# Kernel optimization log

Measured on AMD Instinct MI355X. Metric: run time of the kernel, lower is better.

## Reference

```python
import jax, jax.numpy as jnp
import numpy as np

B, N, NH, E_IN = 2, 2048, 32, 128   # batch, grid cells, neighborhood size, input feat
MD, H, FF, OUT = 512, 8, 2048, 128  # model_dim, heads, ff_dim, output_dim
HD = MD // H                        # head dim = 64
PED, TABLE = 32, 512                # pos_emb_dim, number of (distance,phi) bins
EPS = 1e-5


def setup_inputs() -> dict:
    key = jax.random.key(0)
    ks = jax.random.split(key, 16)
    def w(k, shp, s=0.02):
        return jax.random.normal(k, shp, jnp.float32) * s
    return {
        "x": jax.random.normal(ks[0], (B, N, NH, E_IN), jnp.float32),
        "distances": jax.random.randint(ks[1], (B * N, NH, NH), 0, TABLE),
        "phis": jax.random.randint(ks[2], (B * N, NH, NH), 0, TABLE),
        "W_in": w(ks[3], (E_IN, MD)),
        "dist_table": w(ks[4], (TABLE, PED), 1.0),
        "phi_table": w(ks[5], (TABLE, PED), 1.0),
        "W_bias": w(ks[6], (PED, H)),
        "Wq": w(ks[7], (MD, MD)),
        "Wk": w(ks[8], (MD, MD)),
        "Wv": w(ks[9], (MD, MD)),
        "Wo": w(ks[10], (MD, MD)),
        "W_ff1": w(ks[11], (MD, FF)),
        "W_ff2": w(ks[12], (FF, MD)),
        "g1": jnp.ones((MD,), jnp.float32),
        "b1": jnp.zeros((MD,), jnp.float32),
        "g2": jnp.ones((MD,), jnp.float32),
        "b2": jnp.zeros((MD,), jnp.float32),
        "W_out": w(ks[13], (MD, OUT)),
    }


def _layernorm(x, g, b):
    m = x.mean(-1, keepdims=True)
    v = ((x - m) ** 2).mean(-1, keepdims=True)
    return (x - m) * jax.lax.rsqrt(v + EPS) * g + b


def reference(x, distances, phis, W_in, dist_table, phi_table, W_bias,
              Wq, Wk, Wv, Wo, W_ff1, W_ff2, g1, b1, g2, b2, W_out):
    b, n, nh, _ = x.shape
    m = b * n
    # input_mlp (bias-free Linear), fold (b, n) into batch of attention problems
    h = (x @ W_in).reshape(m, nh, MD)                       # [m, nh, MD]
    # relative position bias: emb_table lookup, product, Linear(PED -> H)
    pe = dist_table[distances] * phi_table[phis]            # [m, nh, nh, PED]
    bias = jnp.einsum('mijp,ph->mhij', pe, W_bias)          # [m, H, nh, nh]
    # MHA with qkv projections (bias-free)
    q = (h @ Wq).reshape(m, nh, H, HD).transpose(0, 2, 1, 3)
    k = (h @ Wk).reshape(m, nh, H, HD).transpose(0, 2, 1, 3)
    v = (h @ Wv).reshape(m, nh, H, HD).transpose(0, 2, 1, 3)
    scores = jnp.einsum('mhid,mhjd->mhij', q, k) / np.sqrt(HD).astype(np.float32)
    att = jax.nn.softmax(scores + bias, axis=-1)            # [m, H, nh, nh]
    o = jnp.einsum('mhij,mhjd->mhid', att, v)
    att_out = o.transpose(0, 2, 1, 3).reshape(m, nh, MD) @ Wo
    # q_res residual (dropout=0), LayerNorm, FFN (SiLU), LayerNorm
    h1 = _layernorm(h + att_out, g1, b1)
    ff = jax.nn.silu(h1 @ W_ff1) @ W_ff2
    h2 = _layernorm(h1 + ff, g2, b2)
    # unfold and output_mlp
    return h2.reshape(b, n, nh, MD) @ W_out                 # [b, n, nh, OUT]
```

## Files before the change

### kernel.cpp

```cpp
#include <hip/hip_runtime.h>
#include <hip/hip_bf16.h>
#include <cstdint>
#include <cstddef>

typedef __bf16 bf16;
typedef __bf16 bf16x8 __attribute__((ext_vector_type(8)));
typedef float  f32x4  __attribute__((ext_vector_type(4)));
typedef float  f32x16 __attribute__((ext_vector_type(16)));

#define DEVI static __device__ __forceinline__

DEVI float ldf(const void* p, size_t i, bool isbf) {
  return isbf ? (float)((const bf16*)p)[i] : ((const float*)p)[i];
}

__global__ void probe_dtype(const void* w, int* flag) {
  int tid = threadIdx.x;
  const bf16* p = (const bf16*)w;
  float mx = 0.f;
  for (int i = tid; i < 2048; i += 64) {
    float v = fabsf((float)p[i]);
    if (!(v < 1e30f)) v = 1e30f;
    mx = fmaxf(mx, v);
  }
#pragma unroll
  for (int d = 32; d; d >>= 1) mx = fmaxf(mx, __shfl_xor(mx, d, 64));
  if (tid == 0) *flag = (mx < 100.f) ? 1 : 0;
}

__global__ void convert_bf16(const void* src, size_t eoff, bf16* dst, int n,
                             const int* flag) {
  int i = (blockIdx.x * 256 + threadIdx.x) * 8;
  if (i >= n) return;
  if (*flag) {
    *(uint4*)(dst + i) = *(const uint4*)((const bf16*)src + eoff + i);
  } else {
    const float* s = (const float*)src + eoff + i;
    float4 a = *(const float4*)s;
    float4 b = *(const float4*)(s + 4);
    bf16 o[8] = {(bf16)a.x, (bf16)a.y, (bf16)a.z, (bf16)a.w,
                 (bf16)b.x, (bf16)b.y, (bf16)b.z, (bf16)b.w};
    *(uint4*)(dst + i) = *(const uint4*)o;
  }
}

__global__ void transpose_w(const void* W, bf16* WT, int K, int N, const int* flag) {
  int idx = blockIdx.x * 256 + threadIdx.x;
  if (idx >= K * N) return;
  int n = idx / K, k = idx - n * K;
  WT[idx] = (bf16)ldf(W, (size_t)k * N + n, *flag != 0);
}

__global__ __launch_bounds__(256) void build_F(const void* dt, const void* pt,
                                               const void* Wb, bf16* F,
                                               const int* flag) {
  int pair = blockIdx.x * 256 + threadIdx.x;
  int d = pair >> 9, ph = pair & 511;
  bool isbf = (*flag != 0);
  float acc[8] = {0, 0, 0, 0, 0, 0, 0, 0};
#pragma unroll
  for (int p = 0; p < 32; ++p) {
    float pe = ldf(dt, (size_t)d * 32 + p, isbf) * ldf(pt, (size_t)ph * 32 + p, isbf);
#pragma unroll
    for (int hh = 0; hh < 8; ++hh) acc[hh] += pe * ldf(Wb, (size_t)p * 8 + hh, isbf);
  }
#pragma unroll
  for (int hh = 0; hh < 8; ++hh) F[(size_t)pair * 8 + hh] = (bf16)acc[hh];
}

__global__ __launch_bounds__(256) void build_bias(const int* __restrict__ dist,
                                                  const int* __restrict__ phi,
                                                  const bf16* __restrict__ F,
                                                  bf16* __restrict__ bias) {
  const int m = blockIdx.x;
#pragma unroll
  for (int it = 0; it < 4; ++it) {
    int e = it * 256 + threadIdx.x;
    int d = dist[(size_t)m * 1024 + e];
    int ph = phi[(size_t)m * 1024 + e];
    uint4 fv = *(const uint4*)(F + ((size_t)d * 512 + ph) * 8);
    const bf16* fe = (const bf16*)&fv;
#pragma unroll
    for (int hh = 0; hh < 8; ++hh)
      bias[((size_t)m * 8 + hh) * 1024 + e] = fe[hh];
  }
}

template <int DO_SILU, int OUT_DUAL>
__global__ __launch_bounds__(256) void gemm_bt(const bf16* __restrict__ A,
                                               const bf16* __restrict__ BT,
                                               void* __restrict__ Cv, int N, int K,
                                               const int* flag, size_t row0) {
  __shared__ bf16 As[128 * 32];
  __shared__ bf16 Bs[128 * 32];
  const int bn = blockIdx.x * 128;
  const int bm = blockIdx.y * 128;
  const int tid = threadIdx.x;
  const int lane = tid & 63;
  const int wave = tid >> 6;
  const int wr = (wave >> 1) * 64, wc = (wave & 1) * 64;
  const int srow = tid >> 2, skk = (tid & 3) * 8;
  const size_t sK = (size_t)K;
  const int kq = (lane >> 4) * 8;
  const int fr = lane & 15;
  f32x4 acc[4][4] = {};
  for (int k0 = 0; k0 < K; k0 += 32) {
    bf16x8 a0 = *(const bf16x8*)(A + (size_t)(bm + srow) * sK + k0 + skk);
    bf16x8 a1 = *(const bf16x8*)(A + (size_t)(bm + 64 + srow) * sK + k0 + skk);
    bf16x8 b0 = *(const bf16x8*)(BT + (size_t)(bn + srow) * sK + k0 + skk);
    bf16x8 b1 = *(const bf16x8*)(BT + (size_t)(bn + 64 + srow) * sK + k0 + skk);
    __syncthreads();
    *(bf16x8*)(As + srow * 32 + skk) = a0;
    *(bf16x8*)(As + (64 + srow) * 32 + skk) = a1;
    *(bf16x8*)(Bs + srow * 32 + skk) = b0;
    *(bf16x8*)(Bs + (64 + srow) * 32 + skk) = b1;
    __syncthreads();
    bf16x8 af[4], bfr[4];
#pragma unroll
    for (int i = 0; i < 4; ++i)
      af[i] = *(const bf16x8*)(As + (wr + i * 16 + fr) * 32 + kq);
#pragma unroll
    for (int j = 0; j < 4; ++j)
      bfr[j] = *(const bf16x8*)(Bs + (wc + j * 16 + fr) * 32 + kq);
#pragma unroll
    for (int i = 0; i < 4; ++i)
#pragma unroll
      for (int j = 0; j < 4; ++j)
        acc[i][j] = __builtin_amdgcn_mfma_f32_16x16x32_bf16(af[i], bfr[j], acc[i][j], 0, 0, 0);
  }
  const int fq = (lane >> 4) * 4;
  const bool write_f32 = OUT_DUAL && flag && (*flag == 0);
#pragma unroll
  for (int i = 0; i < 4; ++i)
#pragma unroll
    for (int j = 0; j < 4; ++j)
#pragma unroll
      for (int r = 0; r < 4; ++r) {
        size_t row = row0 + (size_t)(bm + wr + i * 16 + fq + r);
        size_t col = (size_t)(bn + wc + j * 16 + fr);
        float v = acc[i][j][r];
        if (DO_SILU) v = v / (1.f + __expf(-v));
        if (OUT_DUAL && write_f32)
          ((float*)Cv)[row * N + col] = v;
        else
          ((bf16*)Cv)[row * N + col] = (bf16)v;
      }
}

__global__ __launch_bounds__(512) void attn_fused(const bf16* __restrict__ QKV,
                                                  const bf16* __restrict__ bias,
                                                  bf16* __restrict__ O) {
  const int m = blockIdx.x;
  const int lane = threadIdx.x & 63;
  const int h = threadIdx.x >> 6;
  __shared__ bf16 Vs[8][32 * 64];
  __shared__ bf16 Ps[8][32 * 32];
  const size_t rowbase = (size_t)m * 32 * 1536;
#pragma unroll
  for (int rr = 0; rr < 4; ++rr) {
    int e = rr * 512 + lane * 8;
    int i = e >> 6, c = e & 63;
    *(uint4*)&Vs[h][e] =
        *(const uint4*)(QKV + rowbase + (size_t)i * 1536 + 1024 + h * 64 + c);
  }
  const int fr = lane & 31;
  const int kq = (lane >> 5) * 8;
  bf16x8 qf[4], kf[4];
#pragma unroll
  for (int kk = 0; kk < 4; ++kk) {
    qf[kk] = *(const bf16x8*)(QKV + rowbase + (size_t)fr * 1536 + h * 64 + kk * 16 + kq);
    kf[kk] = *(const bf16x8*)(QKV + rowbase + (size_t)fr * 1536 + 512 + h * 64 + kk * 16 + kq);
  }
  f32x16 s = {};
#pragma unroll
  for (int kk = 0; kk < 4; ++kk)
    s = __builtin_amdgcn_mfma_f32_32x32x16_bf16(qf[kk], kf[kk], s, 0, 0, 0);
  const bf16* bp = bias + ((size_t)m * 8 + h) * 1024;
  const int ri = 4 * (lane >> 5);
  float p[16];
#pragma unroll
  for (int r = 0; r < 16; ++r) {
    int i = (r & 3) + 8 * (r >> 2) + ri;
    p[r] = s[r] * 0.125f + (float)bp[i * 32 + fr];
  }
#pragma unroll
  for (int r = 0; r < 16; ++r) {
    float mx = p[r];
#pragma unroll
    for (int d = 16; d; d >>= 1) mx = fmaxf(mx, __shfl_xor(mx, d, 64));
    float e = __expf(p[r] - mx);
    float sum = e;
#pragma unroll
    for (int d = 16; d; d >>= 1) sum += __shfl_xor(sum, d, 64);
    p[r] = e / sum;
  }
#pragma unroll
  for (int r = 0; r < 16; ++r) {
    int i = (r & 3) + 8 * (r >> 2) + ri;
    Ps[h][i * 32 + fr] = (bf16)p[r];
  }
  __syncthreads();
  bf16x8 pf[2];
#pragma unroll
  for (int kk = 0; kk < 2; ++kk)
    pf[kk] = *(const bf16x8*)(&Ps[h][fr * 32 + kk * 16 + kq]);
  f32x16 o0 = {}, o1 = {};
#pragma unroll
  for (int kk = 0; kk < 2; ++kk) {
    bf16x8 v0, v1;
#pragma unroll
    for (int e = 0; e < 8; ++e) {
      v0[e] = Vs[h][(kk * 16 + kq + e) * 64 + fr];
      v1[e] = Vs[h][(kk * 16 + kq + e) * 64 + 32 + fr];
    }
    o0 = __builtin_amdgcn_mfma_f32_32x32x16_bf16(pf[kk], v0, o0, 0, 0, 0);
    o1 = __builtin_amdgcn_mfma_f32_32x32x16_bf16(pf[kk], v1, o1, 0, 0, 0);
  }
  bf16* op = O + (size_t)m * 32 * 512 + h * 64;
#pragma unroll
  for (int r = 0; r < 16; ++r) {
    int i = (r & 3) + 8 * (r >> 2) + ri;
    op[(size_t)i * 512 + fr] = (bf16)o0[r];
    op[(size_t)i * 512 + 32 + fr] = (bf16)o1[r];
  }
}

__global__ __launch_bounds__(256) void ln_fused(const bf16* __restrict__ X,
                                                const bf16* __restrict__ Y,
                                                const bf16* __restrict__ gb, int gboff,
                                                bf16* __restrict__ out) {
  const int row = blockIdx.x * 4 + (threadIdx.x >> 6);
  const int lane = threadIdx.x & 63;
  uint4 xr = *(const uint4*)(X + (size_t)row * 512 + lane * 8);
  uint4 yr = *(const uint4*)(Y + (size_t)row * 512 + lane * 8);
  const bf16* xe = (const bf16*)&xr;
  const bf16* ye = (const bf16*)&yr;
  float v[8];
  float sum = 0.f;
#pragma unroll
  for (int e = 0; e < 8; ++e) { v[e] = (float)xe[e] + (float)ye[e]; sum += v[e]; }
#pragma unroll
  for (int d = 32; d; d >>= 1) sum += __shfl_xor(sum, d, 64);
  float mean = sum * (1.f / 512.f);
  float var = 0.f;
#pragma unroll
  for (int e = 0; e < 8; ++e) { float t = v[e] - mean; var += t * t; }
#pragma unroll
  for (int d = 32; d; d >>= 1) var += __shfl_xor(var, d, 64);
  float rstd = rsqrtf(var * (1.f / 512.f) + 1e-5f);
  uint4 gr = *(const uint4*)(gb + gboff + lane * 8);
  uint4 br = *(const uint4*)(gb + gboff + 512 + lane * 8);
  const bf16* ge = (const bf16*)&gr;
  const bf16* be = (const bf16*)&br;
  bf16 o[8];
#pragma unroll
  for (int e = 0; e < 8; ++e)
    o[e] = (bf16)((v[e] - mean) * rstd * (float)ge[e] + (float)be[e]);
  *(uint4*)(out + (size_t)row * 512 + lane * 8) = *(const uint4*)o;
}

extern "C" void kernel_launch(void* const* d_in, const int* in_sizes, int n_in,
                              void* d_out, int out_size, void* d_ws, size_t ws_size,
                              hipStream_t stream) {
  const int T = 131072;
  const void* x    = d_in[0];
  const int*  dist = (const int*)d_in[1];
  const int*  phiI = (const int*)d_in[2];
  const void* Win  = d_in[3];
  const void* dtab = d_in[4];
  const void* ptab = d_in[5];
  const void* Wb   = d_in[6];
  const void* Wq   = d_in[7];
  const void* Wk   = d_in[8];
  const void* Wv   = d_in[9];
  const void* Wo   = d_in[10];
  const void* Wf1  = d_in[11];
  const void* Wf2  = d_in[12];
  const void* g1   = d_in[13];
  const void* b1   = d_in[14];
  const void* g2   = d_in[15];
  const void* b2   = d_in[16];
  const void* Wout = d_in[17];
  (void)in_sizes; (void)n_in; (void)out_size;

  const size_t FIXED = (size_t)16 << 20;
  int R = 131072;
  while (R > 1024 && FIXED + (size_t)R * 7936 > ws_size) R >>= 1;
  const int MC = R / 32;
  const int NCHUNK = T / R;

  char* wsb = (char*)d_ws;
  size_t off = 0;
  auto alloc = [&](size_t bytes) {
    char* p = wsb + off;
    off += (bytes + 511) & ~(size_t)511;
    return p;
  };
  int*  flag = (int*)alloc(4);
  bf16* gb   = (bf16*)alloc(2048 * 2);
  bf16* WinT = (bf16*)alloc((size_t)512 * 128 * 2);
  bf16* QKVT = (bf16*)alloc((size_t)1536 * 512 * 2);
  bf16* WoT  = (bf16*)alloc((size_t)512 * 512 * 2);
  bf16* Wf1T = (bf16*)alloc((size_t)2048 * 512 * 2);
  bf16* Wf2T = (bf16*)alloc((size_t)512 * 2048 * 2);
  bf16* WouT = (bf16*)alloc((size_t)128 * 512 * 2);
  bf16* Ftab = (bf16*)alloc((size_t)262144 * 8 * 2);
  bf16* Xc   = (bf16*)alloc((size_t)R * 128 * 2);
  bf16* Hc   = (bf16*)alloc((size_t)R * 512 * 2);
  bf16* big  = (bf16*)alloc((size_t)R * 2048 * 2);
  bf16* Oc   = (bf16*)alloc((size_t)R * 512 * 2);
  bf16* AOc  = (bf16*)alloc((size_t)R * 512 * 2);
  bf16* biasc= (bf16*)alloc((size_t)MC * 8 * 1024 * 2);

  probe_dtype<<<1, 64, 0, stream>>>(Win, flag);
  convert_bf16<<<1, 256, 0, stream>>>(g1, 0, gb + 0, 512, flag);
  convert_bf16<<<1, 256, 0, stream>>>(b1, 0, gb + 512, 512, flag);
  convert_bf16<<<1, 256, 0, stream>>>(g2, 0, gb + 1024, 512, flag);
  convert_bf16<<<1, 256, 0, stream>>>(b2, 0, gb + 1536, 512, flag);
  transpose_w<<<(512 * 128 + 255) / 256, 256, 0, stream>>>(Win, WinT, 128, 512, flag);
  transpose_w<<<(512 * 512 + 255) / 256, 256, 0, stream>>>(Wq, QKVT, 512, 512, flag);
  transpose_w<<<(512 * 512 + 255) / 256, 256, 0, stream>>>(Wk, QKVT + 512 * 512, 512, 512, flag);
  transpose_w<<<(512 * 512 + 255) / 256, 256, 0, stream>>>(Wv, QKVT + 1024 * 512, 512, 512, flag);
  transpose_w<<<(512 * 512 + 255) / 256, 256, 0, stream>>>(Wo, WoT, 512, 512, flag);
  transpose_w<<<(2048 * 512 + 255) / 256, 256, 0, stream>>>(Wf1, Wf1T, 512, 2048, flag);
  transpose_w<<<(2048 * 512 + 255) / 256, 256, 0, stream>>>(Wf2, Wf2T, 2048, 512, flag);
  transpose_w<<<(128 * 512 + 255) / 256, 256, 0, stream>>>(Wout, WouT, 512, 128, flag);
  build_F<<<262144 / 256, 256, 0, stream>>>(dtab, ptab, Wb, Ftab, flag);

  dim3 blk(256);
  for (int c = 0; c < NCHUNK; ++c) {
    const size_t rowoff = (size_t)c * R;
    const size_t moff = (size_t)c * MC;
    convert_bf16<<<(R * 128 / 8 + 255) / 256, 256, 0, stream>>>(x, rowoff * 128, Xc, R * 128, flag);
    gemm_bt<0, 0><<<dim3(4, R / 128), blk, 0, stream>>>(Xc, WinT, Hc, 512, 128, nullptr, 0);
    gemm_bt<0, 0><<<dim3(12, R / 128), blk, 0, stream>>>(Hc, QKVT, big, 1536, 512, nullptr, 0);
    build_bias<<<MC, 256, 0, stream>>>(dist + moff * 1024, phiI + moff * 1024, Ftab, biasc);
    attn_fused<<<MC, 512, 0, stream>>>(big, biasc, Oc);
    gemm_bt<0, 0><<<dim3(4, R / 128), blk, 0, stream>>>(Oc, WoT, AOc, 512, 512, nullptr, 0);
    ln_fused<<<R / 4, 256, 0, stream>>>(Hc, AOc, gb, 0, Hc);
    gemm_bt<1, 0><<<dim3(16, R / 128), blk, 0, stream>>>(Hc, Wf1T, big, 2048, 512, nullptr, 0);
    gemm_bt<0, 0><<<dim3(4, R / 128), blk, 0, stream>>>(big, Wf2T, AOc, 512, 2048, nullptr, 0);
    ln_fused<<<R / 4, 256, 0, stream>>>(Hc, AOc, gb, 1024, Hc);
    gemm_bt<0, 1><<<dim3(1, R / 128), blk, 0, stream>>>(Hc, WouT, d_out, 128, 512, flag, rowoff);
  }
}
```

Before: 2.219 ms.

## Use direct global-to-LDS loads in GEMM and vectorize bias table build

The GEMM tile staging now uses global_load_lds to move A/B tiles straight into shared memory, skipping the register round-trip. The LDS layout relies on tid*8 matching srow*32+skk, which holds. Separately, build_F now reads from pre-converted fp32 tables through float4 loads, caches W_bias in LDS and writes packed 16-byte outputs. The GEMM is still single-buffered with two barriers per K step, so load latency stays exposed.

After: 2.216 ms. Within noise of the previous version (-0.1%).

```diff
diff --git a/kernel.cpp b/kernel.cpp
--- a/kernel.cpp
+++ b/kernel.cpp
@@ -9,6 +9,13 @@
 typedef float  f32x16 __attribute__((ext_vector_type(16)));
 
 #define DEVI static __device__ __forceinline__
+
+DEVI void gload_lds16(const void* g, void* l) {
+  __builtin_amdgcn_global_load_lds(
+      (const __attribute__((address_space(1))) uint32_t*)(uintptr_t)g,
+      (__attribute__((address_space(3))) uint32_t*)(uint32_t)(uintptr_t)l,
+      16, 0, 0);
+}
 
 DEVI float ldf(const void* p, size_t i, bool isbf) {
   return isbf ? (float)((const bf16*)p)[i] : ((const float*)p)[i];
@@ -44,6 +51,12 @@
   }
 }
 
+__global__ void convert_f32(const void* src, float* dst, int n, const int* flag) {
+  int i = blockIdx.x * 256 + threadIdx.x;
+  if (i >= n) return;
+  dst[i] = ldf(src, i, *flag != 0);
+}
+
 __global__ void transpose_w(const void* W, bf16* WT, int K, int N, const int* flag) {
   int idx = blockIdx.x * 256 + threadIdx.x;
   if (idx >= K * N) return;
@@ -51,21 +64,31 @@
   WT[idx] = (bf16)ldf(W, (size_t)k * N + n, *flag != 0);
 }
 
-__global__ __launch_bounds__(256) void build_F(const void* dt, const void* pt,
-                                               const void* Wb, bf16* F,
-                                               const int* flag) {
+__global__ __launch_bounds__(256) void build_F(const float* __restrict__ dt32,
+                                               const float* __restrict__ pt32,
+                                               const float* __restrict__ Wb32,
+                                               bf16* __restrict__ F) {
+  __shared__ float WbS[256];
+  WbS[threadIdx.x] = Wb32[threadIdx.x];
+  __syncthreads();
   int pair = blockIdx.x * 256 + threadIdx.x;
   int d = pair >> 9, ph = pair & 511;
-  bool isbf = (*flag != 0);
+  const float4* dtv = (const float4*)(dt32 + (size_t)d * 32);
+  const float4* ptv = (const float4*)(pt32 + (size_t)ph * 32);
   float acc[8] = {0, 0, 0, 0, 0, 0, 0, 0};
 #pragma unroll
-  for (int p = 0; p < 32; ++p) {
-    float pe = ldf(dt, (size_t)d * 32 + p, isbf) * ldf(pt, (size_t)ph * 32 + p, isbf);
-#pragma unroll
-    for (int hh = 0; hh < 8; ++hh) acc[hh] += pe * ldf(Wb, (size_t)p * 8 + hh, isbf);
-  }
-#pragma unroll
-  for (int hh = 0; hh < 8; ++hh) F[(size_t)pair * 8 + hh] = (bf16)acc[hh];
+  for (int q = 0; q < 8; ++q) {
+    float4 a = dtv[q], b = ptv[q];
+    float pe[4] = {a.x * b.x, a.y * b.y, a.z * b.z, a.w * b.w};
+#pragma unroll
+    for (int e = 0; e < 4; ++e)
+#pragma unroll
+      for (int hh = 0; hh < 8; ++hh) acc[hh] += pe[e] * WbS[(q * 4 + e) * 8 + hh];
+  }
+  bf16 o[8];
+#pragma unroll
+  for (int hh = 0; hh < 8; ++hh) o[hh] = (bf16)acc[hh];
+  *(uint4*)(F + (size_t)pair * 8) = *(const uint4*)o;
 }
 
 __global__ __launch_bounds__(256) void build_bias(const int* __restrict__ dist,
@@ -105,15 +128,11 @@
   const int fr = lane & 15;
   f32x4 acc[4][4] = {};
   for (int k0 = 0; k0 < K; k0 += 32) {
-    bf16x8 a0 = *(const bf16x8*)(A + (size_t)(bm + srow) * sK + k0 + skk);
-    bf16x8 a1 = *(const bf16x8*)(A + (size_t)(bm + 64 + srow) * sK + k0 + skk);
-    bf16x8 b0 = *(const bf16x8*)(BT + (size_t)(bn + srow) * sK + k0 + skk);
-    bf16x8 b1 = *(const bf16x8*)(BT + (size_t)(bn + 64 + srow) * sK + k0 + skk);
     __syncthreads();
-    *(bf16x8*)(As + srow * 32 + skk) = a0;
-    *(bf16x8*)(As + (64 + srow) * 32 + skk) = a1;
-    *(bf16x8*)(Bs + srow * 32 + skk) = b0;
-    *(bf16x8*)(Bs + (64 + srow) * 32 + skk) = b1;
+    gload_lds16(A + (size_t)(bm + srow) * sK + k0 + skk, As + tid * 8);
+    gload_lds16(A + (size_t)(bm + 64 + srow) * sK + k0 + skk, As + 2048 + tid * 8);
+    gload_lds16(BT + (size_t)(bn + srow) * sK + k0 + skk, Bs + tid * 8);
+    gload_lds16(BT + (size_t)(bn + 64 + srow) * sK + k0 + skk, Bs + 2048 + tid * 8);
     __syncthreads();
     bf16x8 af[4], bfr[4];
 #pragma unroll
@@ -298,6 +317,9 @@
   };
   int*  flag = (int*)alloc(4);
   bf16* gb   = (bf16*)alloc(2048 * 2);
+  float* dt32 = (float*)alloc((size_t)512 * 32 * 4);
+  float* pt32 = (float*)alloc((size_t)512 * 32 * 4);
+  float* Wb32 = (float*)alloc(256 * 4);
   bf16* WinT = (bf16*)alloc((size_t)512 * 128 * 2);
   bf16* QKVT = (bf16*)alloc((size_t)1536 * 512 * 2);
   bf16* WoT  = (bf16*)alloc((size_t)512 * 512 * 2);
@@ -317,6 +339,9 @@
   convert_bf16<<<1, 256, 0, stream>>>(b1, 0, gb + 512, 512, flag);
   convert_bf16<<<1, 256, 0, stream>>>(g2, 0, gb + 1024, 512, flag);
   convert_bf16<<<1, 256, 0, stream>>>(b2, 0, gb + 1536, 512, flag);
+  convert_f32<<<64, 256, 0, stream>>>(dtab, dt32, 512 * 32, flag);
+  convert_f32<<<64, 256, 0, stream>>>(ptab, pt32, 512 * 32, flag);
+  convert_f32<<<1, 256, 0, stream>>>(Wb, Wb32, 256, flag);
   transpose_w<<<(512 * 128 + 255) / 256, 256, 0, stream>>>(Win, WinT, 128, 512, flag);
   transpose_w<<<(512 * 512 + 255) / 256, 256, 0, stream>>>(Wq, QKVT, 512, 512, flag);
   transpose_w<<<(512 * 512 + 255) / 256, 256, 0, stream>>>(Wk, QKVT + 512 * 512, 512, 512, flag);
@@ -325,7 +350,7 @@
   transpose_w<<<(2048 * 512 + 255) / 256, 256, 0, stream>>>(Wf1, Wf1T, 512, 2048, flag);
   transpose_w<<<(2048 * 512 + 255) / 256, 256, 0, stream>>>(Wf2, Wf2T, 2048, 512, flag);
   transpose_w<<<(128 * 512 + 255) / 256, 256, 0, stream>>>(Wout, WouT, 512, 128, flag);
-  build_F<<<262144 / 256, 256, 0, stream>>>(dtab, ptab, Wb, Ftab, flag);
+  build_F<<<262144 / 256, 256, 0, stream>>>(dt32, pt32, Wb32, Ftab);
 
   dim3 blk(256);
   for (int c = 0; c < NCHUNK; ++c) {
```
